# Kernel optimization log

Measured on AMD Instinct MI355X. Metric: run time of the kernel, lower is better.

## Reference

```python
import jax, jax.numpy as jnp
import numpy as np

N_NODES = 100000
N_EDGES = 1600000
IN_F = 128
HID_F = 128
OUT_F = 128

def _glorot(key, shape):
    lim = np.sqrt(6.0 / (shape[0] + shape[1]))
    return jax.random.uniform(key, shape, jnp.float32, -lim, lim)

def setup_inputs() -> dict:
    key = jax.random.key(0)
    ks = jax.random.split(key, 9)
    x = jax.random.normal(ks[0], (N_NODES, IN_F), jnp.float32)
    src = jax.random.randint(ks[1], (N_EDGES,), 0, N_NODES, jnp.int32)
    dst = jax.random.randint(ks[2], (N_EDGES,), 0, N_NODES, jnp.int32)
    return {
        'x': x, 'src': src, 'dst': dst,
        'W_self1': _glorot(ks[3], (IN_F, HID_F)),
        'W_neigh1': _glorot(ks[4], (IN_F, HID_F)),
        'b1': jnp.zeros((HID_F,), jnp.float32),
        'W_self2': _glorot(ks[5], (HID_F, OUT_F)),
        'W_neigh2': _glorot(ks[6], (HID_F, OUT_F)),
        'b2': jnp.zeros((OUT_F,), jnp.float32),
    }

def _sage_mean(h, src, dst, W_self, W_neigh, b, n_nodes):
    # mean-aggregate src features onto dst (DGL SAGEConv 'mean')
    msg_sum = jax.ops.segment_sum(h[src], dst, num_segments=n_nodes)  # [N, d]
    deg = jax.ops.segment_sum(jnp.ones_like(dst, jnp.float32), dst, num_segments=n_nodes)
    h_neigh = msg_sum / jnp.maximum(deg, 1.0)[:, None]
    return h @ W_self + h_neigh @ W_neigh + b

def reference(x, src, dst, W_self1, W_neigh1, b1, W_self2, W_neigh2, b2):
    n = x.shape[0]
    h = _sage_mean(x, src, dst, W_self1, W_neigh1, b1, n)
    h = _sage_mean(h, src, dst, W_self2, W_neigh2, b2, n)
    # edge-wise dot product score between endpoint features (u_dot_v)
    s = jnp.sum(h[src] * h[dst], axis=-1)  # [E]
    smin, smax = jnp.min(s), jnp.max(s)
    return (s - smin) / (smax - smin)
```

## Files before the change

### kernel.cpp

```cpp
#include <hip/hip_runtime.h>
#include <hip/hip_bf16.h>

#define F 128

typedef unsigned int uint;
typedef unsigned short ushort;
typedef __attribute__((ext_vector_type(8))) short short8;
typedef __attribute__((ext_vector_type(4))) float f32x4;
typedef __attribute__((ext_vector_type(4))) uint uint4v;

__device__ inline ushort f2bf(float f) {
    uint u = __float_as_uint(f);
    u += 0x7FFF + ((u >> 16) & 1);
    return (ushort)(u >> 16);
}
__device__ inline float2 bf2f(uint u) {
    return make_float2(__uint_as_float(u << 16), __uint_as_float(u & 0xFFFF0000u));
}

__global__ __launch_bounds__(256) void rank_prep(const int* __restrict__ dst,
                                                 int* __restrict__ cnt,
                                                 ushort* __restrict__ rel, int E, int nbE,
                                                 const float* __restrict__ x,
                                                 const float* __restrict__ W0,
                                                 const float* __restrict__ W1,
                                                 const float* __restrict__ W2,
                                                 const float* __restrict__ W3,
                                                 uint* __restrict__ xb,
                                                 ushort* __restrict__ Wt, int NF4) {
    int b = blockIdx.x;
    if (b < nbE) {
        int e = b * 256 + threadIdx.x;
        if (e < E) rel[e] = (ushort)atomicAdd(&cnt[dst[e]], 1);
        return;
    }
    int i = (b - nbE) * 256 + threadIdx.x;
    if (i < NF4) {
        uint4v u = __builtin_nontemporal_load(((const uint4v*)x) + i);
        uint ua = (uint)f2bf(__uint_as_float(u.x)) | ((uint)f2bf(__uint_as_float(u.y)) << 16);
        uint ub = (uint)f2bf(__uint_as_float(u.z)) | ((uint)f2bf(__uint_as_float(u.w)) << 16);
        ((uint2*)xb)[i] = make_uint2(ua, ub);
    } else {
        int idx = i - NF4;
        if (idx >= 4 * 16384) return;
        int j    = idx & 7;
        int lane = (idx >> 3) & 63;
        int t    = (idx >> 9) & 7;
        int kk   = (idx >> 12) & 3;
        int mat  = idx >> 14;
        int n = 16 * t + (lane & 15);
        int k = 32 * kk + 8 * (lane >> 4) + j;
        const float* W = (mat == 0) ? W0 : (mat == 1) ? W1 : (mat == 2) ? W2 : W3;
        Wt[idx] = f2bf(W[k * 128 + n]);
    }
}

__global__ __launch_bounds__(256) void scan_block(const int* __restrict__ cnt,
                                                  int* __restrict__ off,
                                                  int* __restrict__ bsum, int N) {
    __shared__ int t[256];
    int i = blockIdx.x * 256 + threadIdx.x;
    int v = (i < N) ? cnt[i] : 0;
    t[threadIdx.x] = v;
    __syncthreads();
    for (int o = 1; o < 256; o <<= 1) {
        int x = (threadIdx.x >= o) ? t[threadIdx.x - o] : 0;
        __syncthreads();
        t[threadIdx.x] += x;
        __syncthreads();
    }
    if (i < N) off[i] = t[threadIdx.x] - v;
    if (threadIdx.x == 255) bsum[blockIdx.x] = t[255];
}

__global__ __launch_bounds__(512) void scan_sums(int* __restrict__ bsum, int nb) {
    __shared__ int t[512];
    int v = (threadIdx.x < nb) ? bsum[threadIdx.x] : 0;
    t[threadIdx.x] = v;
    __syncthreads();
    for (int o = 1; o < 512; o <<= 1) {
        int x = (threadIdx.x >= o) ? t[threadIdx.x - o] : 0;
        __syncthreads();
        t[threadIdx.x] += x;
        __syncthreads();
    }
    if (threadIdx.x < nb) bsum[threadIdx.x] = t[threadIdx.x] - v;
}

__global__ __launch_bounds__(256) void scan_add_rdeg(int* __restrict__ off,
                                                     const int* __restrict__ bsum,
                                                     const int* __restrict__ cnt,
                                                     float* __restrict__ rdeg, int N) {
    int i = blockIdx.x * 256 + threadIdx.x;
    if (i >= N) return;
    off[i] += bsum[blockIdx.x];
    rdeg[i] = 1.0f / fmaxf((float)cnt[i], 1.0f);
}

__global__ __launch_bounds__(256) void fill_kernel(const int* __restrict__ src,
                                                   const int* __restrict__ dst,
                                                   const int* __restrict__ off,
                                                   const ushort* __restrict__ rel,
                                                   int* __restrict__ srcS, int E) {
    int e = blockIdx.x * 256 + threadIdx.x;
    if (e >= E) return;
    srcS[off[dst[e]] + (int)rel[e]] = src[e];
}

__global__ __launch_bounds__(256) void agg_gather(const uint* __restrict__ hb,
                                                  const int* __restrict__ off,
                                                  const int* __restrict__ srcS,
                                                  const float* __restrict__ rdeg,
                                                  uint* __restrict__ msgb, int N, int E) {
    int node = blockIdx.x * 4 + (threadIdx.x >> 6);
    int lane = threadIdx.x & 63;
    if (node >= N) return;
    int p = off[node];
    int pe = (node == N - 1) ? E : off[node + 1];
    float2 acc = make_float2(0.f, 0.f);
    if (p < pe) {
        int deg = pe - p;
        int last = pe - 1;
        for (; p < pe; p += 16) {
            int s[16];
#pragma unroll
            for (int j = 0; j < 16; j++) s[j] = srcS[min(p + j, last)];
            float2 f[16];
#pragma unroll
            for (int j = 0; j < 16; j++) f[j] = bf2f(hb[(size_t)s[j] * 64 + lane]);
            float2 t0 = make_float2(0.f, 0.f), t1 = make_float2(0.f, 0.f);
#pragma unroll
            for (int j = 0; j < 8; j++) {
                t0.x += f[j].x;       t0.y += f[j].y;
                t1.x += f[j + 8].x;   t1.y += f[j + 8].y;
            }
            acc.x += t0.x + t1.x;
            acc.y += t0.y + t1.y;
        }
        int d = (16 - (deg & 15)) & 15;
        if (d) {
            float2 fl = bf2f(hb[(size_t)srcS[last] * 64 + lane]);
            float fd = (float)d;
            acc.x -= fd * fl.x;
            acc.y -= fd * fl.y;
        }
    }
    float rd = rdeg[node];
    uint w = (uint)f2bf(acc.x * rd) | ((uint)f2bf(acc.y * rd) << 16);
    __builtin_nontemporal_store(w, msgb + (size_t)node * 64 + lane);
}

__global__ __launch_bounds__(256) void sage_mfma(const uint* __restrict__ hb,
                                                 const uint* __restrict__ mb,
                                                 const uint* __restrict__ Wt,
                                                 const float* __restrict__ bias,
                                                 ushort* __restrict__ outb, int N) {
    int wave = threadIdx.x >> 6, lane = threadIdx.x & 63;
    int m = lane & 15, q = lane >> 4;
    int r0 = blockIdx.x * 64 + wave * 16;
    int arow = r0 + m;
    if (arow >= N) arow = N - 1;

    f32x4 acc[8];
#pragma unroll
    for (int t = 0; t < 8; t++) acc[t] = (f32x4){0.f, 0.f, 0.f, 0.f};

    const uint* hrow = hb + (size_t)arow * 64;
    const uint* mrow = mb + (size_t)arow * 64;
#pragma unroll
    for (int sel = 0; sel < 2; sel++) {
        const uint* wsel = Wt + sel * 8192;
#pragma unroll
        for (int kk = 0; kk < 4; kk++) {
            int ko = kk * 16 + q * 4;
            short8 a = sel ? __builtin_nontemporal_load((const short8*)(mrow + ko))
                           : *(const short8*)(hrow + ko);
#pragma unroll
            for (int t = 0; t < 8; t++) {
                short8 b = *(const short8*)(wsel + (size_t)((kk * 8 + t) * 64 + lane) * 4);
                acc[t] = __builtin_amdgcn_mfma_f32_16x16x32_bf16(a, b, acc[t], 0, 0, 0);
            }
        }
    }

#pragma unroll
    for (int t = 0; t < 8; t++) {
        float bs = bias[16 * t + m];
#pragma unroll
        for (int r = 0; r < 4; r++) {
            int orow = r0 + q * 4 + r;
            if (orow < N) outb[(size_t)orow * 128 + 16 * t + m] = f2bf(acc[t][r] + bs);
        }
    }
}

__global__ __launch_bounds__(256) void edge_score_mfma(const uint* __restrict__ hb,
                                                       const int* __restrict__ off,
                                                       const int* __restrict__ srcS,
                                                       float* __restrict__ sc,
                                                       float2* __restrict__ pmm, int N, int E) {
    int node = blockIdx.x * 4 + (threadIdx.x >> 6);
    int lane = threadIdx.x & 63;
    int m = lane & 15, q = lane >> 4;
    float lmin = INFINITY, lmax = -INFINITY;

    if (node < N) {
        int p = off[node];
        int pe = (node == N - 1) ? E : off[node + 1];
        if (p < pe) {
            const uint* nrow = hb + (size_t)node * 64;
            short8 bfr[4];
#pragma unroll
            for (int kk = 0; kk < 4; kk++)
                bfr[kk] = *(const short8*)(nrow + kk * 16 + q * 4);

            for (; p < pe; p += 16) {
                int idx = p + m;
                if (idx >= pe) idx = pe - 1;
                const uint* arow = hb + (size_t)srcS[idx] * 64;
                f32x4 acc = (f32x4){0.f, 0.f, 0.f, 0.f};
#pragma unroll
                for (int kk = 0; kk < 4; kk++) {
                    short8 a = *(const short8*)(arow + kk * 16 + q * 4);
                    acc = __builtin_amdgcn_mfma_f32_16x16x32_bf16(a, bfr[kk], acc, 0, 0, 0);
                }
                if (m == 0) {
                    if (p + 16 <= pe) {
                        *(float4*)(sc + p + q * 4) = make_float4(acc[0], acc[1], acc[2], acc[3]);
                        float mn = fminf(fminf(acc[0], acc[1]), fminf(acc[2], acc[3]));
                        float mx = fmaxf(fmaxf(acc[0], acc[1]), fmaxf(acc[2], acc[3]));
                        lmin = fminf(lmin, mn);
                        lmax = fmaxf(lmax, mx);
                    } else {
#pragma unroll
                        for (int r = 0; r < 4; r++) {
                            int e = p + q * 4 + r;
                            if (e < pe) {
                                sc[e] = acc[r];
                                lmin = fminf(lmin, acc[r]);
                                lmax = fmaxf(lmax, acc[r]);
                            }
                        }
                    }
                }
            }
        }
    }

#pragma unroll
    for (int o = 1; o <= 32; o <<= 1) {
        lmin = fminf(lmin, __shfl_xor(lmin, o));
        lmax = fmaxf(lmax, __shfl_xor(lmax, o));
    }
    __shared__ float smin[4], smax[4];
    int wv = threadIdx.x >> 6;
    if (lane == 0) { smin[wv] = lmin; smax[wv] = lmax; }
    __syncthreads();
    if (threadIdx.x == 0) {
        float mA = fminf(fminf(smin[0], smin[1]), fminf(smin[2], smin[3]));
        float MA = fmaxf(fmaxf(smax[0], smax[1]), fmaxf(smax[2], smax[3]));
        pmm[blockIdx.x] = make_float2(mA, MA);
    }
}

__global__ __launch_bounds__(1024) void minmax_final(const float2* __restrict__ pmm,
                                                     float* __restrict__ mmf, int nb) {
    float vmin = INFINITY, vmax = -INFINITY;
    for (int i = threadIdx.x; i < nb; i += 1024) {
        float2 v = pmm[i];
        vmin = fminf(vmin, v.x);
        vmax = fmaxf(vmax, v.y);
    }
#pragma unroll
    for (int o = 1; o <= 32; o <<= 1) {
        vmin = fminf(vmin, __shfl_xor(vmin, o));
        vmax = fmaxf(vmax, __shfl_xor(vmax, o));
    }
    __shared__ float smin[16], smax[16];
    int lane = threadIdx.x & 63, wv = threadIdx.x >> 6;
    if (lane == 0) { smin[wv] = vmin; smax[wv] = vmax; }
    __syncthreads();
    if (threadIdx.x == 0) {
        float m = smin[0], M = smax[0];
        for (int w = 1; w < 16; w++) { m = fminf(m, smin[w]); M = fmaxf(M, smax[w]); }
        mmf[0] = m;
        mmf[1] = M;
    }
}

__global__ __launch_bounds__(256) void norm_kernel(const float* __restrict__ sc,
                                                   const int* __restrict__ dst,
                                                   const ushort* __restrict__ rel,
                                                   const int* __restrict__ off,
                                                   float* __restrict__ out,
                                                   const float* __restrict__ mmf, int E) {
    float mn = mmf[0];
    float mx = mmf[1];
    float inv = 1.0f / (mx - mn);
    int i = blockIdx.x * 256 + threadIdx.x;
    if (i < E) {
        int p = off[dst[i]] + (int)rel[i];
        out[i] = (sc[p] - mn) * inv;
    }
}

extern "C" void kernel_launch(void* const* d_in, const int* in_sizes, int n_in,
                              void* d_out, int out_size, void* d_ws, size_t ws_size,
                              hipStream_t stream) {
    const float* x   = (const float*)d_in[0];
    const int*   src = (const int*)d_in[1];
    const int*   dst = (const int*)d_in[2];
    const float* Ws1 = (const float*)d_in[3];
    const float* Wn1 = (const float*)d_in[4];
    const float* b1  = (const float*)d_in[5];
    const float* Ws2 = (const float*)d_in[6];
    const float* Wn2 = (const float*)d_in[7];
    const float* b2  = (const float*)d_in[8];

    int N = in_sizes[0] / F;
    int E = in_sizes[1];
    float* out = (float*)d_out;

    int nbN = (N + 255) / 256;
    int nbE = (E + 255) / 256;
    int nbEdgeBlocks = (N + 3) / 4;
    int NF4 = N * F / 4;

    int* off  = (int*)d_ws;
    int* cnt  = off + N;
    int* srcS = cnt + N;
    ushort* rel = (ushort*)(srcS + E);
    float* sc = (float*)((int*)rel + E / 2);
    int* bsum = (int*)(sc + E);
    float* rdeg = (float*)(bsum + 1024);
    float* mmf = (float*)(rdeg + N);
    float2* pmm = (float2*)(mmf + 4);
    uint* Wtb = (uint*)(pmm + 25600);
    size_t elemOff = 3 * (size_t)N + 2 * (size_t)E + (size_t)E / 2 + 1024 + 4 + 51200 + 32768;
    elemOff = (elemOff + 3) & ~(size_t)3;
    uint* xb   = (uint*)d_ws + elemOff;
    uint* msgb = xb + (size_t)N * 64;
    uint* h1b  = msgb + (size_t)N * 64;
    uint* h2b  = h1b + (size_t)N * 64;

    (void)hipMemsetAsync(cnt, 0, (size_t)N * sizeof(int), stream);

    int nbPrep = (NF4 + 4 * 16384 + 255) / 256;
    rank_prep<<<nbE + nbPrep, 256, 0, stream>>>(dst, cnt, rel, E, nbE,
                                                x, Ws1, Wn1, Ws2, Wn2, xb, (ushort*)Wtb, NF4);
    scan_block<<<nbN, 256, 0, stream>>>(cnt, off, bsum, N);
    scan_sums<<<1, 512, 0, stream>>>(bsum, nbN);
    scan_add_rdeg<<<nbN, 256, 0, stream>>>(off, bsum, cnt, rdeg, N);
    fill_kernel<<<nbE, 256, 0, stream>>>(src, dst, off, rel, srcS, E);

    agg_gather<<<(N + 3) / 4, 256, 0, stream>>>(xb, off, srcS, rdeg, msgb, N, E);
    sage_mfma<<<(N + 63) / 64, 256, 0, stream>>>(xb, msgb, Wtb, b1, (ushort*)h1b, N);

    agg_gather<<<(N + 3) / 4, 256, 0, stream>>>(h1b, off, srcS, rdeg, msgb, N, E);
    sage_mfma<<<(N + 63) / 64, 256, 0, stream>>>(h1b, msgb, Wtb + 16384, b2, (ushort*)h2b, N);

    edge_score_mfma<<<nbEdgeBlocks, 256, 0, stream>>>(h2b, off, srcS, sc, pmm, N, E);
    minmax_final<<<1, 1024, 0, stream>>>(pmm, mmf, nbEdgeBlocks);
    norm_kernel<<<(E + 255) / 256, 256, 0, stream>>>(sc, dst, rel, off, out, mmf, E);
}
```

Baseline: 543.7 us.

## Shard degree counters, fold block-sum scan, scatter scores by original edge id

Degree counting now spreads its atomics over 8 counter copies chosen by block index, which cuts contention on hot destination counters. Each slot gets its own per-shard base offset. The separate block-sum scan kernel is removed, and each block now sums the preceding block totals itself. The CSR fill also records the original edge id, so the edge-score kernel writes scores straight to their final positions and normalization becomes a plain vectorized pass with no extra indirection. In exchange it uses 16N more workspace ints, adds an eidS array, and turns coalesced score stores into scattered ones.

After: 571.2 us. 5.1% more time.

```diff
diff --git a/kernel.cpp b/kernel.cpp
--- a/kernel.cpp
+++ b/kernel.cpp
@@ -19,7 +19,7 @@
 }
 
 __global__ __launch_bounds__(256) void rank_prep(const int* __restrict__ dst,
-                                                 int* __restrict__ cnt,
+                                                 int* __restrict__ cnt8,
                                                  ushort* __restrict__ rel, int E, int nbE,
                                                  const float* __restrict__ x,
                                                  const float* __restrict__ W0,
@@ -27,11 +27,11 @@
                                                  const float* __restrict__ W2,
                                                  const float* __restrict__ W3,
                                                  uint* __restrict__ xb,
-                                                 ushort* __restrict__ Wt, int NF4) {
+                                                 ushort* __restrict__ Wt, int NF4, int N) {
     int b = blockIdx.x;
     if (b < nbE) {
         int e = b * 256 + threadIdx.x;
-        if (e < E) rel[e] = (ushort)atomicAdd(&cnt[dst[e]], 1);
+        if (e < E) rel[e] = (ushort)atomicAdd(&cnt8[(size_t)(b & 7) * N + dst[e]], 1);
         return;
     }
     int i = (b - nbE) * 256 + threadIdx.x;
@@ -55,12 +55,16 @@
     }
 }
 
-__global__ __launch_bounds__(256) void scan_block(const int* __restrict__ cnt,
+__global__ __launch_bounds__(256) void scan_block(const int* __restrict__ cnt8,
                                                   int* __restrict__ off,
                                                   int* __restrict__ bsum, int N) {
     __shared__ int t[256];
     int i = blockIdx.x * 256 + threadIdx.x;
-    int v = (i < N) ? cnt[i] : 0;
+    int v = 0;
+    if (i < N) {
+#pragma unroll
+        for (int s = 0; s < 8; s++) v += cnt8[(size_t)s * N + i];
+    }
     t[threadIdx.x] = v;
     __syncthreads();
     for (int o = 1; o < 256; o <<= 1) {
@@ -73,38 +77,49 @@
     if (threadIdx.x == 255) bsum[blockIdx.x] = t[255];
 }
 
-__global__ __launch_bounds__(512) void scan_sums(int* __restrict__ bsum, int nb) {
-    __shared__ int t[512];
-    int v = (threadIdx.x < nb) ? bsum[threadIdx.x] : 0;
-    t[threadIdx.x] = v;
-    __syncthreads();
-    for (int o = 1; o < 512; o <<= 1) {
-        int x = (threadIdx.x >= o) ? t[threadIdx.x - o] : 0;
-        __syncthreads();
-        t[threadIdx.x] += x;
-        __syncthreads();
-    }
-    if (threadIdx.x < nb) bsum[threadIdx.x] = t[threadIdx.x] - v;
-}
-
 __global__ __launch_bounds__(256) void scan_add_rdeg(int* __restrict__ off,
                                                      const int* __restrict__ bsum,
-                                                     const int* __restrict__ cnt,
+                                                     const int* __restrict__ cnt8,
+                                                     int* __restrict__ base8,
                                                      float* __restrict__ rdeg, int N) {
-    int i = blockIdx.x * 256 + threadIdx.x;
+    int b = blockIdx.x;
+    int acc = 0;
+    for (int i = threadIdx.x; i < b; i += 256) acc += bsum[i];
+#pragma unroll
+    for (int o = 1; o <= 32; o <<= 1) acc += __shfl_xor(acc, o);
+    __shared__ int red[4];
+    int wv = threadIdx.x >> 6, ln = threadIdx.x & 63;
+    if (ln == 0) red[wv] = acc;
+    __syncthreads();
+    int prefix = red[0] + red[1] + red[2] + red[3];
+
+    int i = b * 256 + threadIdx.x;
     if (i >= N) return;
-    off[i] += bsum[blockIdx.x];
-    rdeg[i] = 1.0f / fmaxf((float)cnt[i], 1.0f);
+    int o2 = off[i] + prefix;
+    off[i] = o2;
+    int running = o2, tot = 0;
+#pragma unroll
+    for (int s = 0; s < 8; s++) {
+        base8[(size_t)s * N + i] = running;
+        int c = cnt8[(size_t)s * N + i];
+        running += c;
+        tot += c;
+    }
+    rdeg[i] = 1.0f / fmaxf((float)tot, 1.0f);
 }
 
 __global__ __launch_bounds__(256) void fill_kernel(const int* __restrict__ src,
                                                    const int* __restrict__ dst,
-                                                   const int* __restrict__ off,
+                                                   const int* __restrict__ base8,
                                                    const ushort* __restrict__ rel,
-                                                   int* __restrict__ srcS, int E) {
+                                                   int* __restrict__ srcS,
+                                                   int* __restrict__ eidS, int N, int E) {
+    int s = blockIdx.x & 7;
     int e = blockIdx.x * 256 + threadIdx.x;
     if (e >= E) return;
-    srcS[off[dst[e]] + (int)rel[e]] = src[e];
+    int p = base8[(size_t)s * N + dst[e]] + (int)rel[e];
+    srcS[p] = src[e];
+    eidS[p] = e;
 }
 
 __global__ __launch_bounds__(256) void agg_gather(const uint* __restrict__ hb,
@@ -197,6 +212,7 @@
 __global__ __launch_bounds__(256) void edge_score_mfma(const uint* __restrict__ hb,
                                                        const int* __restrict__ off,
                                                        const int* __restrict__ srcS,
+                                                       const int* __restrict__ eidS,
                                                        float* __restrict__ sc,
                                                        float2* __restrict__ pmm, int N, int E) {
     int node = blockIdx.x * 4 + (threadIdx.x >> 6);
@@ -226,7 +242,11 @@
                 }
                 if (m == 0) {
                     if (p + 16 <= pe) {
-                        *(float4*)(sc + p + q * 4) = make_float4(acc[0], acc[1], acc[2], acc[3]);
+                        int4 eid = *(const int4*)(eidS + p + q * 4);
+                        sc[eid.x] = acc[0];
+                        sc[eid.y] = acc[1];
+                        sc[eid.z] = acc[2];
+                        sc[eid.w] = acc[3];
                         float mn = fminf(fminf(acc[0], acc[1]), fminf(acc[2], acc[3]));
                         float mx = fmaxf(fmaxf(acc[0], acc[1]), fmaxf(acc[2], acc[3]));
                         lmin = fminf(lmin, mn);
@@ -236,7 +256,7 @@
                         for (int r = 0; r < 4; r++) {
                             int e = p + q * 4 + r;
                             if (e < pe) {
-                                sc[e] = acc[r];
+                                sc[eidS[e]] = acc[r];
                                 lmin = fminf(lmin, acc[r]);
                                 lmax = fmaxf(lmax, acc[r]);
                             }
@@ -288,20 +308,19 @@
     }
 }
 
-__global__ __launch_bounds__(256) void norm_kernel(const float* __restrict__ sc,
-                                                   const int* __restrict__ dst,
-                                                   const ushort* __restrict__ rel,
-                                                   const int* __restrict__ off,
-                                                   float* __restrict__ out,
-                                                   const float* __restrict__ mmf, int E) {
+__global__ __launch_bounds__(256) void norm4_kernel(const float* __restrict__ sc,
+                                                    float* __restrict__ out,
+                                                    const float* __restrict__ mmf, int E4) {
+    int i = blockIdx.x * 256 + threadIdx.x;
+    if (i >= E4) return;
     float mn = mmf[0];
-    float mx = mmf[1];
-    float inv = 1.0f / (mx - mn);
-    int i = blockIdx.x * 256 + threadIdx.x;
-    if (i < E) {
-        int p = off[dst[i]] + (int)rel[i];
-        out[i] = (sc[p] - mn) * inv;
-    }
+    float inv = 1.0f / (mmf[1] - mn);
+    float4 v = ((const float4*)sc)[i];
+    v.x = (v.x - mn) * inv;
+    v.y = (v.y - mn) * inv;
+    v.z = (v.z - mn) * inv;
+    v.w = (v.w - mn) * inv;
+    ((float4*)out)[i] = v;
 }
 
 extern "C" void kernel_launch(void* const* d_in, const int* in_sizes, int n_in,
@@ -326,32 +345,34 @@
     int nbEdgeBlocks = (N + 3) / 4;
     int NF4 = N * F / 4;
 
-    int* off  = (int*)d_ws;
-    int* cnt  = off + N;
-    int* srcS = cnt + N;
-    ushort* rel = (ushort*)(srcS + E);
+    int* off   = (int*)d_ws;
+    int* cnt8  = off + N;
+    int* base8 = cnt8 + 8 * (size_t)N;
+    int* srcS  = base8 + 8 * (size_t)N;
+    int* eidS  = srcS + E;
+    ushort* rel = (ushort*)(eidS + E);
     float* sc = (float*)((int*)rel + E / 2);
     int* bsum = (int*)(sc + E);
     float* rdeg = (float*)(bsum + 1024);
     float* mmf = (float*)(rdeg + N);
     float2* pmm = (float2*)(mmf + 4);
     uint* Wtb = (uint*)(pmm + 25600);
-    size_t elemOff = 3 * (size_t)N + 2 * (size_t)E + (size_t)E / 2 + 1024 + 4 + 51200 + 32768;
+    size_t elemOff = 18 * (size_t)N + 3 * (size_t)E + (size_t)E / 2 + 1024 + 4 + 51200 + 32768;
     elemOff = (elemOff + 3) & ~(size_t)3;
     uint* xb   = (uint*)d_ws + elemOff;
     uint* msgb = xb + (size_t)N * 64;
     uint* h1b  = msgb + (size_t)N * 64;
     uint* h2b  = h1b + (size_t)N * 64;
 
-    (void)hipMemsetAsync(cnt, 0, (size_t)N * sizeof(int), stream);
+    (void)hipMemsetAsync(cnt8, 0, 8 * (size_t)N * sizeof(int), stream);
 
     int nbPrep = (NF4 + 4 * 16384 + 255) / 256;
-    rank_prep<<<nbE + nbPrep, 256, 0, stream>>>(dst, cnt, rel, E, nbE,
-                                                x, Ws1, Wn1, Ws2, Wn2, xb, (ushort*)Wtb, NF4);
-    scan_block<<<nbN, 256, 0, stream>>>(cnt, off, bsum, N);
-    scan_sums<<<1, 512, 0, stream>>>(bsum, nbN);
-    scan_add_rdeg<<<nbN, 256, 0, stream>>>(off, bsum, cnt, rdeg, N);
-    fill_kernel<<<nbE, 256, 0, stream>>>(src, dst, off, rel, srcS, E);
+    rank_prep<<<nbE + nbPrep, 256, 0, stream>>>(dst, cnt8, rel, E, nbE,
+                                                x, Ws1, Wn1, Ws2, Wn2, xb, (ushort*)Wtb,
+                                                NF4, N);
+    scan_block<<<nbN, 256, 0, stream>>>(cnt8, off, bsum, N);
+    scan_add_rdeg<<<nbN, 256, 0, stream>>>(off, bsum, cnt8, base8, rdeg, N);
+    fill_kernel<<<nbE, 256, 0, stream>>>(src, dst, base8, rel, srcS, eidS, N, E);
 
     agg_gather<<<(N + 3) / 4, 256, 0, stream>>>(xb, off, srcS, rdeg, msgb, N, E);
     sage_mfma<<<(N + 63) / 64, 256, 0, stream>>>(xb, msgb, Wtb, b1, (ushort*)h1b, N);
@@ -359,7 +380,7 @@
     agg_gather<<<(N + 3) / 4, 256, 0, stream>>>(h1b, off, srcS, rdeg, msgb, N, E);
     sage_mfma<<<(N + 63) / 64, 256, 0, stream>>>(h1b, msgb, Wtb + 16384, b2, (ushort*)h2b, N);
 
-    edge_score_mfma<<<nbEdgeBlocks, 256, 0, stream>>>(h2b, off, srcS, sc, pmm, N, E);
+    edge_score_mfma<<<nbEdgeBlocks, 256, 0, stream>>>(h2b, off, srcS, eidS, sc, pmm, N, E);
     minmax_final<<<1, 1024, 0, stream>>>(pmm, mmf, nbEdgeBlocks);
-    norm_kernel<<<(E + 255) / 256, 256, 0, stream>>>(sc, dst, rel, off, out, mmf, E);
-}
+    norm4_kernel<<<(E / 4 + 255) / 256, 256, 0, stream>>>(sc, out, mmf, E / 4);
+}
```
